# Optimization experiments

Measured on AMD Instinct MI355X. Metric: run time of the kernel, lower is better.

## Reference

```python
import jax, jax.numpy as jnp
import numpy as np
from itertools import combinations

A = 4          # anchor_points
K = 16         # neighbor_num
INTRA = A * (A - 1) // 2   # 6
CH = INTRA * 2 + A * A     # 28 = generator channels
B, N, S = 1, 8192, 4096
CIN, COUT = 64, 128


def cdist(x):
    # pairwise euclidean distances [B,N,N], zero-safe sqrt (zero grad at d=0)
    sq = jnp.sum(x * x, -1)
    d2 = sq[:, :, None] + sq[:, None, :] - 2.0 * jnp.einsum('bnc,bmc->bnm', x, x)
    d2 = jnp.maximum(d2, 0.0)
    m = d2 > 0
    return jnp.where(m, jnp.sqrt(jnp.where(m, d2, 1.0)), 0.0)


def index_points(points, idx):
    # points [B,N,...], idx [B,*] -> [B,*,...]
    return jax.vmap(lambda p, i: p[i])(points, idx)


def index_points_dists(dists, i1, i2):
    # dists [B,N,N]; result[b,...] = dists[b, i1[b,...], i2[b,...]]
    i1, i2 = jnp.broadcast_arrays(i1, i2)
    return jax.vmap(lambda d, a, b: d[a, b])(dists, i1, i2)


def generator(xyz):
    # RotationInvariantDistFea.forward(xyz, concat_raw_relative_fea=True)
    D = cdist(xyz)
    neg_nd, ni = jax.lax.top_k(-D, K)   # K >= A; smallest-K, sorted ascending
    nd = -neg_nd
    ai = ni[:, :, :A]
    # intra-anchor dists: dists to anchors 1..A-1 plus pairwise dists among them
    subs = [index_points_dists(D, ai[:, :, pi], ai[:, :, pj])[:, :, None]
            for pi, pj in combinations(range(1, A), 2)]
    intra = jnp.concatenate([nd[:, :, 1:A]] + subs, axis=2)  # [B,P,6]
    # inter-anchor dists: center anchors x neighbor anchors -> [B,P,K,A*A]
    nai = index_points(ai, ni)                                # [B,P,K,A]
    inter = index_points_dists(D, ai[:, :, None, :, None],
                               nai[:, :, :, None, :]).reshape(D.shape[0], D.shape[1], K, A * A)
    center = jnp.broadcast_to(intra[:, :, None, :], (intra.shape[0], intra.shape[1], K, INTRA))
    rf = jnp.concatenate([center, index_points(intra, ni), inter], axis=3)  # [B,P,K,28]
    return rf, ni, D


def mlp(x, W, b, g, be, act):
    # Linear + BatchNorm1d (training mode: stats over batch*points) + optional leaky_relu(0.2)
    y = x @ W + b
    mu = jnp.mean(y, (0, 1))
    var = jnp.var(y, (0, 1))
    y = (y - mu) * jax.lax.rsqrt(var + 1e-5) * g + be
    return jax.nn.leaky_relu(y, 0.2) if act else y


def forward(xyz, feature, sample_indexes, Ww, bw, gw, betaw, Wb, bb, gb, betab, Wo, bo, go, betao):
    rf_before, ni_before, D_before = generator(xyz)
    intra_before = rf_before[:, :, 0, :INTRA]
    xyz_s = index_points(xyz, sample_indexes)
    feat = index_points(feature, sample_indexes)
    intra_before = index_points(intra_before, sample_indexes)
    rf_after, ni_after, _ = generator(xyz_s)
    intra_after = rf_after[:, :, 0, :INTRA]
    a_before = index_points(ni_before[:, :, :A], sample_indexes)                  # [B,S,A]
    a_after = jax.vmap(lambda s, a: s[a])(sample_indexes, ni_after[:, :, :A])     # map to global idx
    inter = index_points_dists(D_before, a_before[:, :, :, None],
                               a_after[:, :, None, :]).reshape(B, S, A * A)
    adf = jnp.concatenate([intra_before, intra_after, inter], axis=2)             # [B,S,28]
    w = mlp(adf, Ww, bw, gw, betaw, False)
    bia = mlp(adf, Wb, bb, gb, betab, False)
    feat = jax.nn.leaky_relu(feat * w + bia, 0.2)
    feat = jnp.concatenate([feat, adf], axis=2)                                   # [B,S,92]
    feat = mlp(feat, Wo, bo, go, betao, True)                                     # [B,S,128]
    return xyz_s, feat, rf_after, ni_after


def setup_inputs():
    key = jax.random.key(0)
    ks = jax.random.split(key, 8)
    xyz = jax.random.normal(ks[0], (B, N, 3), jnp.float32)
    feature = jax.random.normal(ks[1], (B, N, CIN), jnp.float32)
    sample_indexes = jnp.stack([jax.random.permutation(jax.random.fold_in(ks[2], i), N)[:S]
                                for i in range(B)]).astype(jnp.int32)

    def lin(k, cin, cout):
        k1, k2 = jax.random.split(k)
        W = jax.random.normal(k1, (cin, cout), jnp.float32) / np.float32(np.sqrt(cin))
        b = jax.random.normal(k2, (cout,), jnp.float32) * 0.01
        return W, b, jnp.ones((cout,), jnp.float32), jnp.zeros((cout,), jnp.float32)

    Ww, bw, gw, betaw = lin(ks[5], CH, CIN)
    Wb, bb, gb, betab = lin(ks[6], CH, CIN)
    Wo, bo, go, betao = lin(ks[7], CH + CIN, COUT)
    return dict(xyz=xyz, feature=feature, sample_indexes=sample_indexes,
                Ww=Ww, bw=bw, gw=gw, betaw=betaw,
                Wb=Wb, bb=bb, gb=gb, betab=betab,
                Wo=Wo, bo=bo, go=go, betao=betao)


def reference(xyz, feature, sample_indexes, Ww, bw, gw, betaw, Wb, bb, gb, betab, Wo, bo, go, betao):
    return forward(xyz, feature, sample_indexes, Ww, bw, gw, betaw, Wb, bb, gb, betab, Wo, bo, go, betao)
```

## Files before the change

### kernel.cpp

```cpp
#include <hip/hip_runtime.h>
#include <hip/hip_bf16.h>
#include <math.h>

#define N_PTS 8192
#define S_PTS 4096
typedef unsigned long long u64;
typedef unsigned u32;

__device__ __forceinline__ float pair_dist_d(const float4 a, const float4 b) {
    double ax = a.x, ay = a.y, az = a.z;
    double bx = b.x, by = b.y, bz = b.z;
    double dx = ax - bx, dy = ay - by, dz = az - bz;
    double d2 = dx * dx + dy * dy + dz * dz;
    return d2 > 0.0 ? (float)sqrt(d2) : 0.0f;
}

__device__ __forceinline__ float d2_f32_gram(const float4 a, const float4 b) {
    float dot = __fadd_rn(__fadd_rn(__fmul_rn(a.x, b.x), __fmul_rn(a.y, b.y)),
                          __fmul_rn(a.z, b.z));
    float d2 = __fsub_rn(__fadd_rn(a.w, b.w), __fmul_rn(2.0f, dot));
    return fmaxf(d2, 0.0f);
}

__device__ __forceinline__ u32 bitonic64_u32(u32 v, int lane) {
#pragma unroll
    for (int k = 2; k <= 64; k <<= 1) {
#pragma unroll
        for (int j2 = k >> 1; j2 >= 1; j2 >>= 1) {
            u32 o = __shfl_xor(v, j2, 64);
            bool keepMin = (((lane & j2) == 0) == ((lane & k) == 0));
            bool less = o < v;
            v = keepMin ? (less ? o : v) : (less ? v : o);
        }
    }
    return v;
}

__device__ __forceinline__ u64 bitonic64_u64(u64 v, int lane) {
#pragma unroll
    for (int k = 2; k <= 64; k <<= 1) {
#pragma unroll
        for (int j2 = k >> 1; j2 >= 1; j2 >>= 1) {
            u64 o = __shfl_xor(v, j2, 64);
            bool keepMin = (((lane & j2) == 0) == ((lane & k) == 0));
            bool less = o < v;
            v = keepMin ? (less ? o : v) : (less ? v : o);
        }
    }
    return v;
}

__global__ __launch_bounds__(256) void stage_kernel(
        const float* __restrict__ xyz, const int* __restrict__ sidx,
        float4* __restrict__ cb, float4* __restrict__ ca,
        int* __restrict__ inv, float* __restrict__ out_xyz_s) {
    int i = blockIdx.x * blockDim.x + threadIdx.x;
    if (i < N_PTS) {
        float x = xyz[i * 3 + 0], y = xyz[i * 3 + 1], z = xyz[i * 3 + 2];
        float sq = __fadd_rn(__fadd_rn(__fmul_rn(x, x), __fmul_rn(y, y)),
                             __fmul_rn(z, z));
        cb[i] = make_float4(x, y, z, sq);
    }
    if (i < S_PTS) {
        int si = sidx[i];
        float x = xyz[si * 3 + 0], y = xyz[si * 3 + 1], z = xyz[si * 3 + 2];
        float sq = __fadd_rn(__fadd_rn(__fmul_rn(x, x), __fmul_rn(y, y)),
                             __fmul_rn(z, z));
        ca[i] = make_float4(x, y, z, sq);
        inv[si] = i;
        out_xyz_s[i * 3 + 0] = x;
        out_xyz_s[i * 3 + 1] = y;
        out_xyz_s[i * 3 + 2] = z;
    }
}

template <int K, bool AFTER>
__device__ u64 cold_ladder(const float4 q, const float4* __restrict__ cb,
                           const int* __restrict__ inv, int lane) {
    u64 L[K];
#pragma unroll
    for (int j = 0; j < K; ++j) L[j] = ~0ull;
    for (int c = lane; c < N_PTS; c += 64) {
        int low = c;
        bool ok = true;
        if (AFTER) { int iv = inv[c]; ok = iv >= 0; low = iv; }
        if (!ok) continue;
        float d2 = d2_f32_gram(q, cb[c]);
        float D = d2 > 0.0f ? __fsqrt_rn(d2) : 0.0f;
        u64 key = ((u64)__float_as_uint(D) << 32) | (u64)(u32)low;
        if (key < L[K - 1]) {
#pragma unroll
            for (int j = K - 1; j >= 1; --j)
                L[j] = (key < L[j - 1]) ? L[j - 1] : ((key < L[j]) ? key : L[j]);
            L[0] = (key < L[0]) ? key : L[0];
        }
    }
    u64 res = ~0ull;
#pragma unroll
    for (int r = 0; r < K; ++r) {
        u64 m = L[0];
#pragma unroll
        for (int off = 32; off >= 1; off >>= 1) {
            u64 o = __shfl_xor(m, off, 64);
            m = (o < m) ? o : m;
        }
        if (lane == r) res = m;
        if (L[0] == m) {
#pragma unroll
            for (int j = 0; j < K - 1; ++j) L[j] = L[j + 1];
            L[K - 1] = ~0ull;
        }
    }
    return res;
}

template <int K>
__device__ u64 finalize_sort(const u64* buf, u32 cnt, int lane) {
    if (cnt <= 64u) {
        u64 v = (lane < (int)cnt) ? buf[lane] : ~0ull;
        return bitonic64_u64(v, lane);
    }
    u64 L0 = ~0ull, L1 = ~0ull, L2 = ~0ull, L3 = ~0ull;
    for (u32 mm = lane; mm < cnt; mm += 64) {
        u64 kk = buf[mm];
        if (kk < L3) {
            if (kk < L1) {
                L3 = L2; L2 = L1;
                if (kk < L0) { L1 = L0; L0 = kk; } else L1 = kk;
            } else {
                if (kk < L2) { L3 = L2; L2 = kk; } else L3 = kk;
            }
        }
    }
    u64 res = ~0ull;
#pragma unroll
    for (int r = 0; r < K; ++r) {
        u64 mr = L0;
#pragma unroll
        for (int off = 32; off >= 1; off >>= 1) {
            u64 o = __shfl_xor(mr, off, 64);
            mr = (o < mr) ? o : mr;
        }
        if (lane == r) res = mr;
        if (L0 == mr) { L0 = L1; L1 = L2; L2 = L3; L3 = ~0ull; }
    }
    return res;
}

__global__ __launch_bounds__(256, 4) void knn_kernel(
        const float4* __restrict__ cb, const float4* __restrict__ ca,
        const int* __restrict__ inv, const int* __restrict__ sidx,
        int* __restrict__ a_before, float* __restrict__ intra_before,
        int* __restrict__ ni_i, float* __restrict__ intra_after,
        float* __restrict__ out_ni) {
    __shared__ u32 smin[4][256];
    __shared__ u64 sbuf[4][256];
    __shared__ u32 staus[4];
    __shared__ u32 stot[2][4];
    int t = threadIdx.x, lane = t & 63, wid = t >> 6;
    int s0 = blockIdx.x * 2, s1 = s0 + 1;
    float4 q0 = cb[sidx[s0]], q1 = cb[sidx[s1]];

    u32 d20[32], d21[32], msk = 0;
    u32 mnA0 = ~0u, mnA1 = ~0u, mnS0 = ~0u, mnS1 = ~0u;
#pragma unroll
    for (int j = 0; j < 32; ++j) {
        int c = t + 256 * j;
        float4 p = cb[c];
        u32 b0 = __float_as_uint(d2_f32_gram(q0, p));
        u32 b1 = __float_as_uint(d2_f32_gram(q1, p));
        d20[j] = b0; d21[j] = b1;
        bool smp = inv[c] >= 0;
        msk |= (u32)smp << j;
        mnA0 = b0 < mnA0 ? b0 : mnA0;
        mnA1 = b1 < mnA1 ? b1 : mnA1;
        mnS0 = (smp && b0 < mnS0) ? b0 : mnS0;
        mnS1 = (smp && b1 < mnS1) ? b1 : mnS1;
    }
    smin[0][t] = mnA0; smin[1][t] = mnA1; smin[2][t] = mnS0; smin[3][t] = mnS1;
    __syncthreads();
    {
        u32 v = smin[wid][lane];
        u32 v2 = smin[wid][lane + 64];  v = v2 < v ? v2 : v;
        v2 = smin[wid][lane + 128];     v = v2 < v ? v2 : v;
        v2 = smin[wid][lane + 192];     v = v2 < v ? v2 : v;
        v = bitonic64_u32(v, lane);
        int kk = (wid < 2) ? 3 : 15;
        if (lane == kk) staus[wid] = v;
    }
    __syncthreads();
    u32 tb0 = staus[0], tb1 = staus[1], ta0 = staus[2], ta1 = staus[3];
    u32 p0 = 0, p1 = 0;
#pragma unroll
    for (int j = 0; j < 32; ++j) {
        u32 sm = (msk >> j) & 1u;
        p0 += ((d20[j] <= tb0) ? 0x10000u : 0u) + ((sm && d20[j] <= ta0) ? 1u : 0u);
        p1 += ((d21[j] <= tb1) ? 0x10000u : 0u) + ((sm && d21[j] <= ta1) ? 1u : 0u);
    }
    u32 x0 = p0, x1 = p1;
#pragma unroll
    for (int off = 1; off < 64; off <<= 1) {
        u32 y0 = __shfl_up(x0, off, 64);
        u32 y1 = __shfl_up(x1, off, 64);
        if (lane >= off) { x0 += y0; x1 += y1; }
    }
    if (lane == 63) { stot[0][wid] = x0; stot[1][wid] = x1; }
    __syncthreads();
    u32 b0s = x0 - p0, b1s = x1 - p1;
    for (int w = 0; w < wid; ++w) { b0s += stot[0][w]; b1s += stot[1][w]; }
    u32 tot0 = stot[0][0] + stot[0][1] + stot[0][2] + stot[0][3];
    u32 tot1 = stot[1][0] + stot[1][1] + stot[1][2] + stot[1][3];
    u32 cntB0 = tot0 >> 16, cntA0 = tot0 & 0xFFFFu;
    u32 cntB1 = tot1 >> 16, cntA1 = tot1 & 0xFFFFu;
    u32 ob0 = b0s >> 16, oa0 = b0s & 0xFFFFu;
    u32 ob1 = b1s >> 16, oa1 = b1s & 0xFFFFu;
#pragma unroll
    for (int j = 0; j < 32; ++j) {
        int c = t + 256 * j;
        u32 sm = (msk >> j) & 1u;
        bool qb0 = d20[j] <= tb0, qa0 = sm && d20[j] <= ta0;
        if (qb0 || qa0) {
            float d2v = __uint_as_float(d20[j]);
            float D = d2v > 0.0f ? __fsqrt_rn(d2v) : 0.0f;
            u64 hk = (u64)__float_as_uint(D) << 32;
            if (qb0 && cntB0 <= 256u) sbuf[0][ob0++] = hk | (u64)(u32)c;
            if (qa0 && cntA0 <= 256u) sbuf[2][oa0++] = hk | (u64)(u32)inv[c];
        }
        bool qb1 = d21[j] <= tb1, qa1 = sm && d21[j] <= ta1;
        if (qb1 || qa1) {
            float d2v = __uint_as_float(d21[j]);
            float D = d2v > 0.0f ? __fsqrt_rn(d2v) : 0.0f;
            u64 hk = (u64)__float_as_uint(D) << 32;
            if (qb1 && cntB1 <= 256u) sbuf[1][ob1++] = hk | (u64)(u32)c;
            if (qa1 && cntA1 <= 256u) sbuf[3][oa1++] = hk | (u64)(u32)inv[c];
        }
    }
    __syncthreads();
    int s = (wid & 1) ? s1 : s0;
    float4 q = (wid & 1) ? q1 : q0;
    u32 cnt = (wid == 0) ? cntB0 : (wid == 1) ? cntB1 : (wid == 2) ? cntA0 : cntA1;
    u64 res;
    if (wid < 2) {
        res = (cnt <= 256u) ? finalize_sort<4>(sbuf[wid], cnt, lane)
                            : cold_ladder<4, false>(q, cb, inv, lane);
        int idx = (int)(res & 0xffffffffull);
        if (lane < 4) a_before[s * 4 + lane] = idx;
        if (lane >= 1 && lane < 4)
            intra_before[s * 6 + (lane - 1)] = pair_dist_d(q, cb[idx]);
        int i1 = __shfl(idx, 1, 64);
        int i2 = __shfl(idx, 2, 64);
        int i3 = __shfl(idx, 3, 64);
        if (lane < 3) {
            int pa = (lane == 2) ? i2 : i1;
            int pb = (lane == 0) ? i2 : i3;
            intra_before[s * 6 + 3 + lane] = pair_dist_d(cb[pa], cb[pb]);
        }
    } else {
        res = (cnt <= 256u) ? finalize_sort<16>(sbuf[wid], cnt, lane)
                            : cold_ladder<16, true>(q, cb, inv, lane);
        int idx = (int)(res & 0xffffffffull);
        if (lane < 16) {
            ni_i[s * 16 + lane] = idx;
            out_ni[s * 16 + lane] = (float)idx;
        }
        if (lane >= 1 && lane < 4)
            intra_after[s * 6 + (lane - 1)] = pair_dist_d(q, ca[idx]);
        int i1 = __shfl(idx, 1, 64);
        int i2 = __shfl(idx, 2, 64);
        int i3 = __shfl(idx, 3, 64);
        if (lane < 3) {
            int pa = (lane == 2) ? i2 : i1;
            int pb = (lane == 0) ? i2 : i3;
            intra_after[s * 6 + 3 + lane] = pair_dist_d(ca[pa], ca[pb]);
        }
    }
}

__global__ __launch_bounds__(256) void asm_mlp1_kernel(
        const float4* __restrict__ ca, const float4* __restrict__ cb,
        const int* __restrict__ ni_i, const float* __restrict__ intra_after,
        const int* __restrict__ a_before, const float* __restrict__ intra_before,
        const int* __restrict__ sidx,
        const float* __restrict__ Ww, const float* __restrict__ bw,
        const float* __restrict__ Wb, const float* __restrict__ bb,
        float* __restrict__ out_rf, float* __restrict__ adf,
        float* __restrict__ y_wb) {
    __shared__ int s_ni[4][16];
    __shared__ float s_rf[4][16 * 28];
    __shared__ float s_ia[4][8];
    __shared__ float s_adf[4][28];
    __shared__ float sW[28 * 128];
    __shared__ float sb[128];
    int t = threadIdx.x, wid = t >> 6, lane = t & 63;
    int s = blockIdx.x * 4 + wid;
    for (int i = t; i < 28 * 128; i += 256) {
        int k = i >> 7, c = i & 127;
        sW[i] = (c < 64) ? Ww[k * 64 + c] : Wb[k * 64 + (c - 64)];
    }
    if (t < 128) sb[t] = (t < 64) ? bw[t] : bb[t - 64];
    if (lane < 16) s_ni[wid][lane] = ni_i[s * 16 + lane];
    if (lane < 6) s_ia[wid][lane] = intra_after[s * 6 + lane];
    __syncthreads();

    int k = lane >> 2, qq = lane & 3;
    int nai_q = ni_i[s_ni[wid][k] * 16 + qq];
    float4 pq = ca[nai_q];
#pragma unroll
    for (int p = 0; p < 4; ++p) {
        float4 pp = ca[s_ni[wid][p]];
        s_rf[wid][k * 28 + 12 + p * 4 + qq] = pair_dist_d(pp, pq);
    }
    for (int idx = lane; idx < 16 * 12; idx += 64) {
        int kk = idx / 12, c = idx % 12;
        float v = (c < 6) ? s_ia[wid][c] : intra_after[s_ni[wid][kk] * 6 + (c - 6)];
        s_rf[wid][kk * 28 + c] = v;
    }
    if (lane < 16) {
        int p = lane >> 2, q2 = lane & 3;
        int ib = a_before[s * 4 + p];
        int ia = sidx[s_ni[wid][q2]];
        float v = pair_dist_d(cb[ib], cb[ia]);
        adf[s * 28 + 12 + lane] = v;
        s_adf[wid][12 + lane] = v;
    } else if (lane >= 32 && lane < 38) {
        float v = intra_before[s * 6 + (lane - 32)];
        adf[s * 28 + (lane - 32)] = v;
        s_adf[wid][lane - 32] = v;
    } else if (lane >= 40 && lane < 46) {
        float v = s_ia[wid][lane - 40];
        adf[s * 28 + 6 + (lane - 40)] = v;
        s_adf[wid][6 + (lane - 40)] = v;
    }
    const int base = s * 16 * 28;
    for (int idx = lane; idx < 16 * 28; idx += 64) out_rf[base + idx] = s_rf[wid][idx];
    __syncthreads();
    int s0 = blockIdx.x * 4;
#pragma unroll
    for (int o = t; o < 512; o += 256) {
        int r = o >> 7, c = o & 127;
        float acc = sb[c];
#pragma unroll
        for (int k2 = 0; k2 < 28; ++k2)
            acc = fmaf(s_adf[r][k2], sW[k2 * 128 + c], acc);
        y_wb[c * 4096 + s0 + r] = acc;
    }
}

__global__ __launch_bounds__(256) void stats_kernel(
        const float* __restrict__ y,
        const float* __restrict__ g0, const float* __restrict__ be0,
        const float* __restrict__ g1, const float* __restrict__ be1, int csplit,
        float* __restrict__ scale, float* __restrict__ shift) {
    int c = blockIdx.x;
    const float* p = y + c * 4096;
    float s1 = 0.0f, s2 = 0.0f;
    for (int i = threadIdx.x; i < 4096; i += 256) {
        float v = p[i];
        s1 += v;
        s2 = fmaf(v, v, s2);
    }
    __shared__ float l1[256], l2[256];
    l1[threadIdx.x] = s1;
    l2[threadIdx.x] = s2;
    __syncthreads();
    for (int off = 128; off; off >>= 1) {
        if (threadIdx.x < off) {
            l1[threadIdx.x] += l1[threadIdx.x + off];
            l2[threadIdx.x] += l2[threadIdx.x + off];
        }
        __syncthreads();
    }
    if (threadIdx.x == 0) {
        float mean = l1[0] * (1.0f / 4096.0f);
        float var = l2[0] * (1.0f / 4096.0f) - mean * mean;
        float g = (c < csplit) ? g0[c] : g1[c - csplit];
        float be = (c < csplit) ? be0[c] : be1[c - csplit];
        float sc = g / sqrtf(var + 1e-5f);
        scale[c] = sc;
        shift[c] = be - mean * sc;
    }
}

__global__ __launch_bounds__(256) void mlp2_kernel(
        const float* __restrict__ y_wb,
        const float* __restrict__ scale1, const float* __restrict__ shift1,
        const float* __restrict__ feature, const int* __restrict__ sidx,
        const float* __restrict__ adf,
        const float* __restrict__ Wo, const float* __restrict__ bo,
        float* __restrict__ y_o) {
    __shared__ float sW[92 * 128];
    __shared__ float t2[16 * 129];
    __shared__ float scat[16 * 92];
    int t = threadIdx.x;
    int s0 = blockIdx.x * 16;
    for (int i = t; i < 92 * 128; i += 256) sW[i] = Wo[i];
    for (int i = t; i < 16 * 128; i += 256) {
        int row = i & 15, c = i >> 4;
        t2[row * 129 + c] = fmaf(y_wb[c * 4096 + s0 + row], scale1[c], shift1[c]);
    }
    __syncthreads();
    for (int rr = 0; rr < 16; rr += 4) {
        int r = rr + (t >> 6);
        int c = t & 63;
        int si = sidx[s0 + r];
        float f = feature[si * 64 + c];
        float v = fmaf(f, t2[r * 129 + c], t2[r * 129 + 64 + c]);
        scat[r * 92 + c] = v >= 0.0f ? v : 0.2f * v;
    }
    for (int i = t; i < 16 * 28; i += 256) {
        int row = i / 28, k = i % 28;
        scat[row * 92 + 64 + k] = adf[(s0 + row) * 28 + k];
    }
    __syncthreads();
    int r = t >> 4, cg = t & 15;
    float acc[8];
#pragma unroll
    for (int j = 0; j < 8; ++j) acc[j] = bo[cg * 8 + j];
    for (int c = 0; c < 92; ++c) {
        float a = scat[r * 92 + c];
#pragma unroll
        for (int j = 0; j < 8; ++j)
            acc[j] = fmaf(a, sW[c * 128 + cg * 8 + j], acc[j]);
    }
    int s = s0 + r;
#pragma unroll
    for (int j = 0; j < 8; ++j) y_o[(cg * 8 + j) * 4096 + s] = acc[j];
}

__global__ __launch_bounds__(256) void final_kernel(
        const float* __restrict__ y_o,
        const float* __restrict__ go, const float* __restrict__ betao,
        float* __restrict__ out_feat) {
    int j = blockIdx.x;
    const float* p = y_o + j * 4096;
    float s1 = 0.0f, s2 = 0.0f;
    for (int i = threadIdx.x; i < 4096; i += 256) {
        float v = p[i];
        s1 += v;
        s2 = fmaf(v, v, s2);
    }
    __shared__ float l1[256], l2[256];
    __shared__ float ssc, ssh;
    l1[threadIdx.x] = s1;
    l2[threadIdx.x] = s2;
    __syncthreads();
    for (int off = 128; off; off >>= 1) {
        if (threadIdx.x < off) {
            l1[threadIdx.x] += l1[threadIdx.x + off];
            l2[threadIdx.x] += l2[threadIdx.x + off];
        }
        __syncthreads();
    }
    if (threadIdx.x == 0) {
        float mean = l1[0] * (1.0f / 4096.0f);
        float var = l2[0] * (1.0f / 4096.0f) - mean * mean;
        float sc = go[j] / sqrtf(var + 1e-5f);
        ssc = sc;
        ssh = betao[j] - mean * sc;
    }
    __syncthreads();
    float sc = ssc, sh = ssh;
    for (int i = threadIdx.x; i < 4096; i += 256) {
        float v = fmaf(p[i], sc, sh);
        v = v >= 0.0f ? v : 0.2f * v;
        out_feat[i * 128 + j] = v;
    }
}

extern "C" void kernel_launch(void* const* d_in, const int* in_sizes, int n_in,
                              void* d_out, int out_size, void* d_ws, size_t ws_size,
                              hipStream_t stream) {
    const float* xyz = (const float*)d_in[0];
    const float* feature = (const float*)d_in[1];
    const int* sidx = (const int*)d_in[2];
    const float* Ww = (const float*)d_in[3];
    const float* bw = (const float*)d_in[4];
    const float* gw = (const float*)d_in[5];
    const float* betaw = (const float*)d_in[6];
    const float* Wb = (const float*)d_in[7];
    const float* bb = (const float*)d_in[8];
    const float* gb = (const float*)d_in[9];
    const float* betab = (const float*)d_in[10];
    const float* Wo = (const float*)d_in[11];
    const float* bo = (const float*)d_in[12];
    const float* go = (const float*)d_in[13];
    const float* betao = (const float*)d_in[14];

    float* out = (float*)d_out;
    float* out_xyz = out;
    float* out_feat = out + 12288;
    float* out_rf = out + 12288 + 524288;
    float* out_ni = out + 12288 + 524288 + 1835008;

    float* ws = (float*)d_ws;
    float4* cb = (float4*)ws;
    float4* ca = (float4*)(ws + 32768);
    int* a_before = (int*)(ws + 49152);
    float* intra_before = ws + 65536;
    int* ni_i = (int*)(ws + 90112);
    float* intra_after = ws + 155648;
    float* adf = ws + 180224;
    float* y_wb = ws + 294912;
    float* y_o = ws + 819200;
    float* scale1 = ws + 1343488;
    float* shift1 = ws + 1343616;
    int* inv = (int*)(ws + 1343744);

    hipMemsetAsync(inv, 0xFF, N_PTS * sizeof(int), stream);
    stage_kernel<<<32, 256, 0, stream>>>(xyz, sidx, cb, ca, inv, out_xyz);
    knn_kernel<<<2048, 256, 0, stream>>>(cb, ca, inv, sidx, a_before, intra_before,
                                         ni_i, intra_after, out_ni);
    asm_mlp1_kernel<<<1024, 256, 0, stream>>>(ca, cb, ni_i, intra_after, a_before,
                                              intra_before, sidx, Ww, bw, Wb, bb,
                                              out_rf, adf, y_wb);
    stats_kernel<<<128, 256, 0, stream>>>(y_wb, gw, betaw, gb, betab, 64, scale1, shift1);
    mlp2_kernel<<<256, 256, 0, stream>>>(y_wb, scale1, shift1, feature, sidx, adf, Wo, bo, y_o);
    final_kernel<<<128, 256, 0, stream>>>(y_o, go, betao, out_feat);
}
```

Baseline: 198.8 us.

## Tile kNN over 8 queries per block and fuse MLP tail into cooperative kernel

The kNN kernel now handles 8 queries per block, staging point tiles in shared memory and recomputing distances in two passes instead of keeping them in registers. Candidates are collected with shared-memory atomics into smaller buffers, which makes the cold fallback more likely to trigger. The four post-kNN kernels are merged into one cooperative kernel with grid-wide syncs, removing launch gaps between them. In exchange, the kNN grid drops to 512 blocks, the distances are computed twice, and the tail runs on only 256 blocks.

```diff
diff --git a/kernel.cpp b/kernel.cpp
--- a/kernel.cpp
+++ b/kernel.cpp
@@ -1,9 +1,14 @@
 #include <hip/hip_runtime.h>
+#include <hip/hip_cooperative_groups.h>
 #include <hip/hip_bf16.h>
 #include <math.h>
 
+namespace cg = cooperative_groups;
+
 #define N_PTS 8192
 #define S_PTS 4096
+#define TILE 2048
+#define CAP 128
 typedef unsigned long long u64;
 typedef unsigned u32;
 
@@ -147,323 +152,332 @@
     return res;
 }
 
-__global__ __launch_bounds__(256, 4) void knn_kernel(
+__global__ __launch_bounds__(256, 2) void knn_kernel(
         const float4* __restrict__ cb, const float4* __restrict__ ca,
         const int* __restrict__ inv, const int* __restrict__ sidx,
         int* __restrict__ a_before, float* __restrict__ intra_before,
         int* __restrict__ ni_i, float* __restrict__ intra_after,
         float* __restrict__ out_ni) {
-    __shared__ u32 smin[4][256];
-    __shared__ u64 sbuf[4][256];
-    __shared__ u32 staus[4];
-    __shared__ u32 stot[2][4];
+    __shared__ float4 tile[TILE];
+    __shared__ int tinv[TILE];
+    __shared__ u32 sminT[2][8][256];
+    __shared__ u32 staus[2][8];
+    __shared__ u32 scnt[2][8];
+    __shared__ u64 sbuf[2][8][CAP];
+    __shared__ float4 sq[8];
+
     int t = threadIdx.x, lane = t & 63, wid = t >> 6;
-    int s0 = blockIdx.x * 2, s1 = s0 + 1;
-    float4 q0 = cb[sidx[s0]], q1 = cb[sidx[s1]];
-
-    u32 d20[32], d21[32], msk = 0;
-    u32 mnA0 = ~0u, mnA1 = ~0u, mnS0 = ~0u, mnS1 = ~0u;
-#pragma unroll
-    for (int j = 0; j < 32; ++j) {
-        int c = t + 256 * j;
-        float4 p = cb[c];
-        u32 b0 = __float_as_uint(d2_f32_gram(q0, p));
-        u32 b1 = __float_as_uint(d2_f32_gram(q1, p));
-        d20[j] = b0; d21[j] = b1;
-        bool smp = inv[c] >= 0;
-        msk |= (u32)smp << j;
-        mnA0 = b0 < mnA0 ? b0 : mnA0;
-        mnA1 = b1 < mnA1 ? b1 : mnA1;
-        mnS0 = (smp && b0 < mnS0) ? b0 : mnS0;
-        mnS1 = (smp && b1 < mnS1) ? b1 : mnS1;
-    }
-    smin[0][t] = mnA0; smin[1][t] = mnA1; smin[2][t] = mnS0; smin[3][t] = mnS1;
+    int s0 = blockIdx.x * 8;
+    if (t < 8) sq[t] = cb[sidx[s0 + t]];
+    if (t < 16) scnt[t >> 3][t & 7] = 0;
     __syncthreads();
-    {
-        u32 v = smin[wid][lane];
-        u32 v2 = smin[wid][lane + 64];  v = v2 < v ? v2 : v;
-        v2 = smin[wid][lane + 128];     v = v2 < v ? v2 : v;
-        v2 = smin[wid][lane + 192];     v = v2 < v ? v2 : v;
+    float4 q[8];
+#pragma unroll
+    for (int i = 0; i < 8; ++i) q[i] = sq[i];
+
+    u32 mB[8], mA[8];
+#pragma unroll
+    for (int i = 0; i < 8; ++i) { mB[i] = ~0u; mA[i] = ~0u; }
+
+    for (int tb = 0; tb < N_PTS; tb += TILE) {
+        __syncthreads();
+        for (int i = t; i < TILE; i += 256) { tile[i] = cb[tb + i]; tinv[i] = inv[tb + i]; }
+        __syncthreads();
+#pragma unroll
+        for (int jj = 0; jj < TILE / 256; ++jj) {
+            int li = t + jj * 256;
+            float4 p = tile[li];
+            bool smp = tinv[li] >= 0;
+#pragma unroll
+            for (int i = 0; i < 8; ++i) {
+                u32 b = __float_as_uint(d2_f32_gram(q[i], p));
+                mB[i] = b < mB[i] ? b : mB[i];
+                if (smp) mA[i] = b < mA[i] ? b : mA[i];
+            }
+        }
+    }
+#pragma unroll
+    for (int i = 0; i < 8; ++i) { sminT[0][i][t] = mB[i]; sminT[1][i][t] = mA[i]; }
+    __syncthreads();
+    for (int m = 0; m < 4; ++m) {
+        int st = wid + m * 4;
+        int k = st >> 3, qi = st & 7;
+        u32 v = sminT[k][qi][lane];
+        u32 v2 = sminT[k][qi][lane + 64];  v = v2 < v ? v2 : v;
+        v2 = sminT[k][qi][lane + 128];     v = v2 < v ? v2 : v;
+        v2 = sminT[k][qi][lane + 192];     v = v2 < v ? v2 : v;
         v = bitonic64_u32(v, lane);
-        int kk = (wid < 2) ? 3 : 15;
-        if (lane == kk) staus[wid] = v;
+        int kk = (k == 0) ? 3 : 15;
+        if (lane == kk) staus[k][qi] = v;
     }
     __syncthreads();
-    u32 tb0 = staus[0], tb1 = staus[1], ta0 = staus[2], ta1 = staus[3];
-    u32 p0 = 0, p1 = 0;
-#pragma unroll
-    for (int j = 0; j < 32; ++j) {
-        u32 sm = (msk >> j) & 1u;
-        p0 += ((d20[j] <= tb0) ? 0x10000u : 0u) + ((sm && d20[j] <= ta0) ? 1u : 0u);
-        p1 += ((d21[j] <= tb1) ? 0x10000u : 0u) + ((sm && d21[j] <= ta1) ? 1u : 0u);
-    }
-    u32 x0 = p0, x1 = p1;
-#pragma unroll
-    for (int off = 1; off < 64; off <<= 1) {
-        u32 y0 = __shfl_up(x0, off, 64);
-        u32 y1 = __shfl_up(x1, off, 64);
-        if (lane >= off) { x0 += y0; x1 += y1; }
-    }
-    if (lane == 63) { stot[0][wid] = x0; stot[1][wid] = x1; }
+    u32 tB[8], tA[8];
+#pragma unroll
+    for (int i = 0; i < 8; ++i) { tB[i] = staus[0][i]; tA[i] = staus[1][i]; }
+
+    for (int tb = 0; tb < N_PTS; tb += TILE) {
+        __syncthreads();
+        for (int i = t; i < TILE; i += 256) { tile[i] = cb[tb + i]; tinv[i] = inv[tb + i]; }
+        __syncthreads();
+#pragma unroll
+        for (int jj = 0; jj < TILE / 256; ++jj) {
+            int li = t + jj * 256;
+            float4 p = tile[li];
+            int iv = tinv[li];
+            bool smp = iv >= 0;
+            int c = tb + li;
+#pragma unroll
+            for (int i = 0; i < 8; ++i) {
+                u32 b = __float_as_uint(d2_f32_gram(q[i], p));
+                bool qb = b <= tB[i];
+                bool qa = smp && (b <= tA[i]);
+                if (qb || qa) {
+                    float d2v = __uint_as_float(b);
+                    float D = d2v > 0.0f ? __fsqrt_rn(d2v) : 0.0f;
+                    u64 hk = (u64)__float_as_uint(D) << 32;
+                    if (qb) {
+                        u32 pos = atomicAdd(&scnt[0][i], 1u);
+                        if (pos < CAP) sbuf[0][i][pos] = hk | (u64)(u32)c;
+                    }
+                    if (qa) {
+                        u32 pos = atomicAdd(&scnt[1][i], 1u);
+                        if (pos < CAP) sbuf[1][i][pos] = hk | (u64)(u32)iv;
+                    }
+                }
+            }
+        }
+    }
     __syncthreads();
-    u32 b0s = x0 - p0, b1s = x1 - p1;
-    for (int w = 0; w < wid; ++w) { b0s += stot[0][w]; b1s += stot[1][w]; }
-    u32 tot0 = stot[0][0] + stot[0][1] + stot[0][2] + stot[0][3];
-    u32 tot1 = stot[1][0] + stot[1][1] + stot[1][2] + stot[1][3];
-    u32 cntB0 = tot0 >> 16, cntA0 = tot0 & 0xFFFFu;
-    u32 cntB1 = tot1 >> 16, cntA1 = tot1 & 0xFFFFu;
-    u32 ob0 = b0s >> 16, oa0 = b0s & 0xFFFFu;
-    u32 ob1 = b1s >> 16, oa1 = b1s & 0xFFFFu;
-#pragma unroll
-    for (int j = 0; j < 32; ++j) {
-        int c = t + 256 * j;
-        u32 sm = (msk >> j) & 1u;
-        bool qb0 = d20[j] <= tb0, qa0 = sm && d20[j] <= ta0;
-        if (qb0 || qa0) {
-            float d2v = __uint_as_float(d20[j]);
-            float D = d2v > 0.0f ? __fsqrt_rn(d2v) : 0.0f;
-            u64 hk = (u64)__float_as_uint(D) << 32;
-            if (qb0 && cntB0 <= 256u) sbuf[0][ob0++] = hk | (u64)(u32)c;
-            if (qa0 && cntA0 <= 256u) sbuf[2][oa0++] = hk | (u64)(u32)inv[c];
-        }
-        bool qb1 = d21[j] <= tb1, qa1 = sm && d21[j] <= ta1;
-        if (qb1 || qa1) {
-            float d2v = __uint_as_float(d21[j]);
-            float D = d2v > 0.0f ? __fsqrt_rn(d2v) : 0.0f;
-            u64 hk = (u64)__float_as_uint(D) << 32;
-            if (qb1 && cntB1 <= 256u) sbuf[1][ob1++] = hk | (u64)(u32)c;
-            if (qa1 && cntA1 <= 256u) sbuf[3][oa1++] = hk | (u64)(u32)inv[c];
-        }
-    }
-    __syncthreads();
-    int s = (wid & 1) ? s1 : s0;
-    float4 q = (wid & 1) ? q1 : q0;
-    u32 cnt = (wid == 0) ? cntB0 : (wid == 1) ? cntB1 : (wid == 2) ? cntA0 : cntA1;
-    u64 res;
-    if (wid < 2) {
-        res = (cnt <= 256u) ? finalize_sort<4>(sbuf[wid], cnt, lane)
-                            : cold_ladder<4, false>(q, cb, inv, lane);
-        int idx = (int)(res & 0xffffffffull);
-        if (lane < 4) a_before[s * 4 + lane] = idx;
-        if (lane >= 1 && lane < 4)
-            intra_before[s * 6 + (lane - 1)] = pair_dist_d(q, cb[idx]);
-        int i1 = __shfl(idx, 1, 64);
-        int i2 = __shfl(idx, 2, 64);
-        int i3 = __shfl(idx, 3, 64);
-        if (lane < 3) {
-            int pa = (lane == 2) ? i2 : i1;
-            int pb = (lane == 0) ? i2 : i3;
-            intra_before[s * 6 + 3 + lane] = pair_dist_d(cb[pa], cb[pb]);
-        }
-    } else {
-        res = (cnt <= 256u) ? finalize_sort<16>(sbuf[wid], cnt, lane)
-                            : cold_ladder<16, true>(q, cb, inv, lane);
-        int idx = (int)(res & 0xffffffffull);
-        if (lane < 16) {
-            ni_i[s * 16 + lane] = idx;
-            out_ni[s * 16 + lane] = (float)idx;
-        }
-        if (lane >= 1 && lane < 4)
-            intra_after[s * 6 + (lane - 1)] = pair_dist_d(q, ca[idx]);
-        int i1 = __shfl(idx, 1, 64);
-        int i2 = __shfl(idx, 2, 64);
-        int i3 = __shfl(idx, 3, 64);
-        if (lane < 3) {
-            int pa = (lane == 2) ? i2 : i1;
-            int pb = (lane == 0) ? i2 : i3;
-            intra_after[s * 6 + 3 + lane] = pair_dist_d(ca[pa], ca[pb]);
-        }
-    }
-}
-
-__global__ __launch_bounds__(256) void asm_mlp1_kernel(
+    for (int m = 0; m < 4; ++m) {
+        int st = wid + m * 4;
+        int k = st >> 3, qi = st & 7;
+        int s = s0 + qi;
+        u32 cnt = scnt[k][qi];
+        float4 qq = q[qi];
+        if (k == 0) {
+            u64 res = (cnt <= CAP) ? finalize_sort<4>(sbuf[0][qi], cnt, lane)
+                                   : cold_ladder<4, false>(qq, cb, inv, lane);
+            int idx = (int)(res & 0xffffffffull);
+            if (lane < 4) a_before[s * 4 + lane] = idx;
+            if (lane >= 1 && lane < 4)
+                intra_before[s * 6 + (lane - 1)] = pair_dist_d(qq, cb[idx]);
+            int i1 = __shfl(idx, 1, 64);
+            int i2 = __shfl(idx, 2, 64);
+            int i3 = __shfl(idx, 3, 64);
+            if (lane < 3) {
+                int pa = (lane == 2) ? i2 : i1;
+                int pb = (lane == 0) ? i2 : i3;
+                intra_before[s * 6 + 3 + lane] = pair_dist_d(cb[pa], cb[pb]);
+            }
+        } else {
+            u64 res = (cnt <= CAP) ? finalize_sort<16>(sbuf[1][qi], cnt, lane)
+                                   : cold_ladder<16, true>(qq, cb, inv, lane);
+            int idx = (int)(res & 0xffffffffull);
+            if (lane < 16) {
+                ni_i[s * 16 + lane] = idx;
+                out_ni[s * 16 + lane] = (float)idx;
+            }
+            if (lane >= 1 && lane < 4)
+                intra_after[s * 6 + (lane - 1)] = pair_dist_d(qq, ca[idx]);
+            int i1 = __shfl(idx, 1, 64);
+            int i2 = __shfl(idx, 2, 64);
+            int i3 = __shfl(idx, 3, 64);
+            if (lane < 3) {
+                int pa = (lane == 2) ? i2 : i1;
+                int pb = (lane == 0) ? i2 : i3;
+                intra_after[s * 6 + 3 + lane] = pair_dist_d(ca[pa], ca[pb]);
+            }
+        }
+    }
+}
+
+struct PhA {
+    float sW1[28 * 128];
+    float sb1[128];
+    int s_ni[4][16];
+    float s_rf[4][448];
+    float s_ia[4][8];
+    float s_adf[16][28];
+};
+struct PhB { float l1[256]; float l2[256]; float sc, sh; };
+struct PhC { float sW[92 * 128]; float t2[16 * 129]; float scat[16 * 92]; };
+union TailU { PhA a; PhB b; PhC c; };
+
+__global__ __launch_bounds__(256) void fused_tail_kernel(
         const float4* __restrict__ ca, const float4* __restrict__ cb,
         const int* __restrict__ ni_i, const float* __restrict__ intra_after,
         const int* __restrict__ a_before, const float* __restrict__ intra_before,
         const int* __restrict__ sidx,
         const float* __restrict__ Ww, const float* __restrict__ bw,
         const float* __restrict__ Wb, const float* __restrict__ bb,
+        const float* __restrict__ gw, const float* __restrict__ betaw,
+        const float* __restrict__ gb, const float* __restrict__ betab,
+        const float* __restrict__ feature,
+        const float* __restrict__ Wo, const float* __restrict__ bo,
+        const float* __restrict__ go, const float* __restrict__ betao,
         float* __restrict__ out_rf, float* __restrict__ adf,
-        float* __restrict__ y_wb) {
-    __shared__ int s_ni[4][16];
-    __shared__ float s_rf[4][16 * 28];
-    __shared__ float s_ia[4][8];
-    __shared__ float s_adf[4][28];
-    __shared__ float sW[28 * 128];
-    __shared__ float sb[128];
+        float* __restrict__ y_wb, float* __restrict__ scale1,
+        float* __restrict__ shift1, float* __restrict__ y_o,
+        float* __restrict__ out_feat) {
+    cg::grid_group grid = cg::this_grid();
+    __shared__ TailU su;
     int t = threadIdx.x, wid = t >> 6, lane = t & 63;
-    int s = blockIdx.x * 4 + wid;
+    int b = blockIdx.x;
+
     for (int i = t; i < 28 * 128; i += 256) {
         int k = i >> 7, c = i & 127;
-        sW[i] = (c < 64) ? Ww[k * 64 + c] : Wb[k * 64 + (c - 64)];
-    }
-    if (t < 128) sb[t] = (t < 64) ? bw[t] : bb[t - 64];
-    if (lane < 16) s_ni[wid][lane] = ni_i[s * 16 + lane];
-    if (lane < 6) s_ia[wid][lane] = intra_after[s * 6 + lane];
+        su.a.sW1[i] = (c < 64) ? Ww[k * 64 + c] : Wb[k * 64 + (c - 64)];
+    }
+    if (t < 128) su.a.sb1[t] = (t < 64) ? bw[t] : bb[t - 64];
     __syncthreads();
-
-    int k = lane >> 2, qq = lane & 3;
-    int nai_q = ni_i[s_ni[wid][k] * 16 + qq];
-    float4 pq = ca[nai_q];
-#pragma unroll
-    for (int p = 0; p < 4; ++p) {
-        float4 pp = ca[s_ni[wid][p]];
-        s_rf[wid][k * 28 + 12 + p * 4 + qq] = pair_dist_d(pp, pq);
-    }
-    for (int idx = lane; idx < 16 * 12; idx += 64) {
-        int kk = idx / 12, c = idx % 12;
-        float v = (c < 6) ? s_ia[wid][c] : intra_after[s_ni[wid][kk] * 6 + (c - 6)];
-        s_rf[wid][kk * 28 + c] = v;
-    }
-    if (lane < 16) {
-        int p = lane >> 2, q2 = lane & 3;
-        int ib = a_before[s * 4 + p];
-        int ia = sidx[s_ni[wid][q2]];
-        float v = pair_dist_d(cb[ib], cb[ia]);
-        adf[s * 28 + 12 + lane] = v;
-        s_adf[wid][12 + lane] = v;
-    } else if (lane >= 32 && lane < 38) {
-        float v = intra_before[s * 6 + (lane - 32)];
-        adf[s * 28 + (lane - 32)] = v;
-        s_adf[wid][lane - 32] = v;
-    } else if (lane >= 40 && lane < 46) {
-        float v = s_ia[wid][lane - 40];
-        adf[s * 28 + 6 + (lane - 40)] = v;
-        s_adf[wid][6 + (lane - 40)] = v;
-    }
-    const int base = s * 16 * 28;
-    for (int idx = lane; idx < 16 * 28; idx += 64) out_rf[base + idx] = s_rf[wid][idx];
-    __syncthreads();
-    int s0 = blockIdx.x * 4;
-#pragma unroll
-    for (int o = t; o < 512; o += 256) {
-        int r = o >> 7, c = o & 127;
-        float acc = sb[c];
+    for (int r = 0; r < 4; ++r) {
+        int s = b * 16 + r * 4 + wid;
+        int slot = r * 4 + wid;
+        if (lane < 16) su.a.s_ni[wid][lane] = ni_i[s * 16 + lane];
+        if (lane < 6) su.a.s_ia[wid][lane] = intra_after[s * 6 + lane];
+        __syncthreads();
+        int k = lane >> 2, qq = lane & 3;
+        int nai_q = ni_i[su.a.s_ni[wid][k] * 16 + qq];
+        float4 pq = ca[nai_q];
+#pragma unroll
+        for (int p = 0; p < 4; ++p) {
+            float4 pp = ca[su.a.s_ni[wid][p]];
+            su.a.s_rf[wid][k * 28 + 12 + p * 4 + qq] = pair_dist_d(pp, pq);
+        }
+        for (int idx = lane; idx < 16 * 12; idx += 64) {
+            int kk = idx / 12, c = idx % 12;
+            float v = (c < 6) ? su.a.s_ia[wid][c]
+                              : intra_after[su.a.s_ni[wid][kk] * 6 + (c - 6)];
+            su.a.s_rf[wid][kk * 28 + c] = v;
+        }
+        if (lane < 16) {
+            int p = lane >> 2, q2 = lane & 3;
+            int ib = a_before[s * 4 + p];
+            int ia = sidx[su.a.s_ni[wid][q2]];
+            float v = pair_dist_d(cb[ib], cb[ia]);
+            adf[s * 28 + 12 + lane] = v;
+            su.a.s_adf[slot][12 + lane] = v;
+        } else if (lane >= 32 && lane < 38) {
+            float v = intra_before[s * 6 + (lane - 32)];
+            adf[s * 28 + (lane - 32)] = v;
+            su.a.s_adf[slot][lane - 32] = v;
+        } else if (lane >= 40 && lane < 46) {
+            float v = su.a.s_ia[wid][lane - 40];
+            adf[s * 28 + 6 + (lane - 40)] = v;
+            su.a.s_adf[slot][6 + (lane - 40)] = v;
+        }
+        const int base = s * 16 * 28;
+        for (int idx = lane; idx < 16 * 28; idx += 64)
+            out_rf[base + idx] = su.a.s_rf[wid][idx];
+        __syncthreads();
+    }
+    int sbase = b * 16;
+    for (int o = t; o < 2048; o += 256) {
+        int r2 = o >> 7, c = o & 127;
+        float acc = su.a.sb1[c];
 #pragma unroll
         for (int k2 = 0; k2 < 28; ++k2)
-            acc = fmaf(s_adf[r][k2], sW[k2 * 128 + c], acc);
-        y_wb[c * 4096 + s0 + r] = acc;
-    }
-}
-
-__global__ __launch_bounds__(256) void stats_kernel(
-        const float* __restrict__ y,
-        const float* __restrict__ g0, const float* __restrict__ be0,
-        const float* __restrict__ g1, const float* __restrict__ be1, int csplit,
-        float* __restrict__ scale, float* __restrict__ shift) {
-    int c = blockIdx.x;
-    const float* p = y + c * 4096;
-    float s1 = 0.0f, s2 = 0.0f;
-    for (int i = threadIdx.x; i < 4096; i += 256) {
-        float v = p[i];
-        s1 += v;
-        s2 = fmaf(v, v, s2);
-    }
-    __shared__ float l1[256], l2[256];
-    l1[threadIdx.x] = s1;
-    l2[threadIdx.x] = s2;
-    __syncthreads();
-    for (int off = 128; off; off >>= 1) {
-        if (threadIdx.x < off) {
-            l1[threadIdx.x] += l1[threadIdx.x + off];
-            l2[threadIdx.x] += l2[threadIdx.x + off];
-        }
-        __syncthreads();
-    }
-    if (threadIdx.x == 0) {
-        float mean = l1[0] * (1.0f / 4096.0f);
-        float var = l2[0] * (1.0f / 4096.0f) - mean * mean;
-        float g = (c < csplit) ? g0[c] : g1[c - csplit];
-        float be = (c < csplit) ? be0[c] : be1[c - csplit];
-        float sc = g / sqrtf(var + 1e-5f);
-        scale[c] = sc;
-        shift[c] = be - mean * sc;
-    }
-}
-
-__global__ __launch_bounds__(256) void mlp2_kernel(
-        const float* __restrict__ y_wb,
-        const float* __restrict__ scale1, const float* __restrict__ shift1,
-        const float* __restrict__ feature, const int* __restrict__ sidx,
-        const float* __restrict__ adf,
-        const float* __restrict__ Wo, const float* __restrict__ bo,
-        float* __restrict__ y_o) {
-    __shared__ float sW[92 * 128];
-    __shared__ float t2[16 * 129];
-    __shared__ float scat[16 * 92];
-    int t = threadIdx.x;
-    int s0 = blockIdx.x * 16;
-    for (int i = t; i < 92 * 128; i += 256) sW[i] = Wo[i];
-    for (int i = t; i < 16 * 128; i += 256) {
-        int row = i & 15, c = i >> 4;
-        t2[row * 129 + c] = fmaf(y_wb[c * 4096 + s0 + row], scale1[c], shift1[c]);
-    }
-    __syncthreads();
-    for (int rr = 0; rr < 16; rr += 4) {
-        int r = rr + (t >> 6);
-        int c = t & 63;
-        int si = sidx[s0 + r];
-        float f = feature[si * 64 + c];
-        float v = fmaf(f, t2[r * 129 + c], t2[r * 129 + 64 + c]);
-        scat[r * 92 + c] = v >= 0.0f ? v : 0.2f * v;
-    }
-    for (int i = t; i < 16 * 28; i += 256) {
-        int row = i / 28, k = i % 28;
-        scat[row * 92 + 64 + k] = adf[(s0 + row) * 28 + k];
-    }
-    __syncthreads();
-    int r = t >> 4, cg = t & 15;
-    float acc[8];
-#pragma unroll
-    for (int j = 0; j < 8; ++j) acc[j] = bo[cg * 8 + j];
-    for (int c = 0; c < 92; ++c) {
-        float a = scat[r * 92 + c];
-#pragma unroll
-        for (int j = 0; j < 8; ++j)
-            acc[j] = fmaf(a, sW[c * 128 + cg * 8 + j], acc[j]);
-    }
-    int s = s0 + r;
-#pragma unroll
-    for (int j = 0; j < 8; ++j) y_o[(cg * 8 + j) * 4096 + s] = acc[j];
-}
-
-__global__ __launch_bounds__(256) void final_kernel(
-        const float* __restrict__ y_o,
-        const float* __restrict__ go, const float* __restrict__ betao,
-        float* __restrict__ out_feat) {
-    int j = blockIdx.x;
-    const float* p = y_o + j * 4096;
-    float s1 = 0.0f, s2 = 0.0f;
-    for (int i = threadIdx.x; i < 4096; i += 256) {
-        float v = p[i];
-        s1 += v;
-        s2 = fmaf(v, v, s2);
-    }
-    __shared__ float l1[256], l2[256];
-    __shared__ float ssc, ssh;
-    l1[threadIdx.x] = s1;
-    l2[threadIdx.x] = s2;
-    __syncthreads();
-    for (int off = 128; off; off >>= 1) {
-        if (threadIdx.x < off) {
-            l1[threadIdx.x] += l1[threadIdx.x + off];
-            l2[threadIdx.x] += l2[threadIdx.x + off];
-        }
-        __syncthreads();
-    }
-    if (threadIdx.x == 0) {
-        float mean = l1[0] * (1.0f / 4096.0f);
-        float var = l2[0] * (1.0f / 4096.0f) - mean * mean;
-        float sc = go[j] / sqrtf(var + 1e-5f);
-        ssc = sc;
-        ssh = betao[j] - mean * sc;
-    }
-    __syncthreads();
-    float sc = ssc, sh = ssh;
-    for (int i = threadIdx.x; i < 4096; i += 256) {
-        float v = fmaf(p[i], sc, sh);
-        v = v >= 0.0f ? v : 0.2f * v;
-        out_feat[i * 128 + j] = v;
+            acc = fmaf(su.a.s_adf[r2][k2], su.a.sW1[k2 * 128 + c], acc);
+        y_wb[c * 4096 + sbase + r2] = acc;
+    }
+    grid.sync();
+
+    if (b < 128) {
+        int c = b;
+        const float* p = y_wb + c * 4096;
+        float s1 = 0.0f, s2 = 0.0f;
+        for (int i = t; i < 4096; i += 256) {
+            float v = p[i];
+            s1 += v;
+            s2 = fmaf(v, v, s2);
+        }
+        su.b.l1[t] = s1;
+        su.b.l2[t] = s2;
+        __syncthreads();
+        for (int off = 128; off; off >>= 1) {
+            if (t < off) { su.b.l1[t] += su.b.l1[t + off]; su.b.l2[t] += su.b.l2[t + off]; }
+            __syncthreads();
+        }
+        if (t == 0) {
+            float mean = su.b.l1[0] * (1.0f / 4096.0f);
+            float var = su.b.l2[0] * (1.0f / 4096.0f) - mean * mean;
+            float g = (c < 64) ? gw[c] : gb[c - 64];
+            float be = (c < 64) ? betaw[c] : betab[c - 64];
+            float sc = g / sqrtf(var + 1e-5f);
+            scale1[c] = sc;
+            shift1[c] = be - mean * sc;
+        }
+    }
+    grid.sync();
+
+    {
+        int s0 = b * 16;
+        for (int i = t; i < 92 * 128; i += 256) su.c.sW[i] = Wo[i];
+        for (int i = t; i < 16 * 128; i += 256) {
+            int row = i & 15, c = i >> 4;
+            su.c.t2[row * 129 + c] =
+                fmaf(y_wb[c * 4096 + s0 + row], scale1[c], shift1[c]);
+        }
+        __syncthreads();
+        for (int rr = 0; rr < 16; rr += 4) {
+            int r = rr + (t >> 6);
+            int c = t & 63;
+            int si = sidx[s0 + r];
+            float f = feature[si * 64 + c];
+            float v = fmaf(f, su.c.t2[r * 129 + c], su.c.t2[r * 129 + 64 + c]);
+            su.c.scat[r * 92 + c] = v >= 0.0f ? v : 0.2f * v;
+        }
+        for (int i = t; i < 16 * 28; i += 256) {
+            int row = i / 28, k = i % 28;
+            su.c.scat[row * 92 + 64 + k] = adf[(s0 + row) * 28 + k];
+        }
+        __syncthreads();
+        int r = t >> 4, cg2 = t & 15;
+        float acc[8];
+#pragma unroll
+        for (int j = 0; j < 8; ++j) acc[j] = bo[cg2 * 8 + j];
+        for (int c = 0; c < 92; ++c) {
+            float a = su.c.scat[r * 92 + c];
+#pragma unroll
+            for (int j = 0; j < 8; ++j)
+                acc[j] = fmaf(a, su.c.sW[c * 128 + cg2 * 8 + j], acc[j]);
+        }
+        int s = s0 + r;
+#pragma unroll
+        for (int j = 0; j < 8; ++j) y_o[(cg2 * 8 + j) * 4096 + s] = acc[j];
+    }
+    grid.sync();
+
+    if (b < 128) {
+        int j = b;
+        const float* p = y_o + j * 4096;
+        float s1 = 0.0f, s2 = 0.0f;
+        for (int i = t; i < 4096; i += 256) {
+            float v = p[i];
+            s1 += v;
+            s2 = fmaf(v, v, s2);
+        }
+        su.b.l1[t] = s1;
+        su.b.l2[t] = s2;
+        __syncthreads();
+        for (int off = 128; off; off >>= 1) {
+            if (t < off) { su.b.l1[t] += su.b.l1[t + off]; su.b.l2[t] += su.b.l2[t + off]; }
+            __syncthreads();
+        }
+        if (t == 0) {
+            float mean = su.b.l1[0] * (1.0f / 4096.0f);
+            float var = su.b.l2[0] * (1.0f / 4096.0f) - mean * mean;
+            float sc = go[j] / sqrtf(var + 1e-5f);
+            su.b.sc = sc;
+            su.b.sh = betao[j] - mean * sc;
+        }
+        __syncthreads();
+        float sc = su.b.sc, sh = su.b.sh;
+        for (int i = t; i < 4096; i += 256) {
+            float v = fmaf(p[i], sc, sh);
+            v = v >= 0.0f ? v : 0.2f * v;
+            out_feat[i * 128 + j] = v;
+        }
     }
 }
 
@@ -508,12 +522,22 @@
 
     hipMemsetAsync(inv, 0xFF, N_PTS * sizeof(int), stream);
     stage_kernel<<<32, 256, 0, stream>>>(xyz, sidx, cb, ca, inv, out_xyz);
-    knn_kernel<<<2048, 256, 0, stream>>>(cb, ca, inv, sidx, a_before, intra_before,
-                                         ni_i, intra_after, out_ni);
-    asm_mlp1_kernel<<<1024, 256, 0, stream>>>(ca, cb, ni_i, intra_after, a_before,
-                                              intra_before, sidx, Ww, bw, Wb, bb,
-                                              out_rf, adf, y_wb);
-    stats_kernel<<<128, 256, 0, stream>>>(y_wb, gw, betaw, gb, betab, 64, scale1, shift1);
-    mlp2_kernel<<<256, 256, 0, stream>>>(y_wb, scale1, shift1, feature, sidx, adf, Wo, bo, y_o);
-    final_kernel<<<128, 256, 0, stream>>>(y_o, go, betao, out_feat);
-}
+    knn_kernel<<<512, 256, 0, stream>>>(cb, ca, inv, sidx, a_before, intra_before,
+                                        ni_i, intra_after, out_ni);
+    {
+        const float4* ca_ = ca; const float4* cb_ = cb;
+        const int* ni_ = ni_i; const float* ia_ = intra_after;
+        const int* ab_ = a_before; const float* ib_ = intra_before;
+        const int* sx_ = sidx;
+        void* args[] = {
+            (void*)&ca_, (void*)&cb_, (void*)&ni_, (void*)&ia_,
+            (void*)&ab_, (void*)&ib_, (void*)&sx_,
+            (void*)&Ww, (void*)&bw, (void*)&Wb, (void*)&bb,
+            (void*)&gw, (void*)&betaw, (void*)&gb, (void*)&betab,
+            (void*)&feature, (void*)&Wo, (void*)&bo, (void*)&go, (void*)&betao,
+            (void*)&out_rf, (void*)&adf, (void*)&y_wb, (void*)&scale1,
+            (void*)&shift1, (void*)&y_o, (void*)&out_feat };
+        hipLaunchCooperativeKernel((const void*)fused_tail_kernel, dim3(256),
+                                   dim3(256), args, 0, stream);
+    }
+}
```

After: 333.6 us. +67.8%, slower.
